# Performance work log

Measured on AMD Instinct MI355X. Metric: run time of the kernel, lower is better.

## Reference

```python
import jax, jax.numpy as jnp
import numpy as np

B, C, L, T = 8, 512, 2048, 64

def setup_inputs() -> dict:
    key = jax.random.key(0)
    k1, k2, k3 = jax.random.split(key, 3)
    x = jax.random.normal(k1, (B, C, 1, L), dtype=jnp.float32)
    W1 = jax.random.normal(k2, (T, C), dtype=jnp.float32) * (1.0 / np.sqrt(C))
    W2 = jax.random.normal(k3, (T, C), dtype=jnp.float32) * (1.0 / np.sqrt(C))
    gamma = jnp.ones((1, 1), dtype=jnp.float32)
    ranges = 0  # unused by forward
    return {"x": x, "W1": W1, "W2": W2, "gamma": gamma, "ranges": ranges}

def reference(x, W1, W2, gamma, ranges):
    temp = x[:, :, 0, :]                                  # (B, C, L)
    q = jnp.einsum('tc,bcl->btl', W1, temp)               # conv1x1 -> (B, T, L)
    k = jnp.einsum('tc,bcl->btl', W2, temp)               # conv1x1 -> (B, T, L)
    scores = jnp.einsum('btl,btm->blm', q, k)             # Q^T K -> (B, L, L)
    attn = jax.nn.softmax(scores, axis=2)                 # softmax over last dim
    # temp @ attn^T: out[:, :, j] = sum_i attn[j, i] * temp[:, :, i]
    out = jnp.einsum('bci,bji->bcj', temp, attn)          # (B, C, L)
    out = temp + gamma[0, 0] * out                        # gamma scale + residual
    return out[:, :, None, :]                             # (B, C, 1, L)
```

## Files before the change

kernel.cpp:

```cpp
#include <hip/hip_runtime.h>
#include <cstddef>

#define BB 8
#define CC 512
#define LL 2048
#define TT 64

typedef short short8 __attribute__((ext_vector_type(8)));
typedef float floatx4 __attribute__((ext_vector_type(4)));
typedef unsigned short b16u;
typedef unsigned int u32;

static __device__ __forceinline__ unsigned f2bfu(float f) {
    unsigned u = __float_as_uint(f);
    u += 0x7fffu + ((u >> 16) & 1u);
    return u >> 16;
}
static __device__ __forceinline__ float bfu2f(unsigned h) {
    return __uint_as_float(h << 16);
}

#define MFMA16(a, b, c) __builtin_amdgcn_mfma_f32_16x16x32_bf16((a), (b), (c), 0, 0, 0)

__global__ __launch_bounds__(256) void wcvt_kernel(
    const float* __restrict__ W1, const float* __restrict__ W2,
    b16u* __restrict__ W1h, b16u* __restrict__ W1l,
    b16u* __restrict__ W2h, b16u* __restrict__ W2l)
{
    int flat = blockIdx.x * 256 + threadIdx.x;
    float4 v1 = *(const float4*)(W1 + (size_t)flat * 4);
    float4 v2 = *(const float4*)(W2 + (size_t)flat * 4);
    const float* e1 = (const float*)&v1;
    const float* e2 = (const float*)&v2;
    unsigned h1[4], l1[4], h2[4], l2[4];
#pragma unroll
    for (int k = 0; k < 4; ++k) {
        h1[k] = f2bfu(e1[k]); l1[k] = f2bfu(e1[k] - bfu2f(h1[k]));
        h2[k] = f2bfu(e2[k]); l2[k] = f2bfu(e2[k] - bfu2f(h2[k]));
    }
    uint2 a, b, c, d;
    a.x = h1[0] | (h1[1] << 16); a.y = h1[2] | (h1[3] << 16);
    b.x = l1[0] | (l1[1] << 16); b.y = l1[2] | (l1[3] << 16);
    c.x = h2[0] | (h2[1] << 16); c.y = h2[2] | (h2[3] << 16);
    d.x = l2[0] | (l2[1] << 16); d.y = l2[2] | (l2[3] << 16);
    *(uint2*)(W1h + (size_t)flat * 4) = a;
    *(uint2*)(W1l + (size_t)flat * 4) = b;
    *(uint2*)(W2h + (size_t)flat * 4) = c;
    *(uint2*)(W2l + (size_t)flat * 4) = d;
}

__global__ __launch_bounds__(256) void qkcvt_kernel(
    const float* __restrict__ x,
    const b16u* __restrict__ W1h, const b16u* __restrict__ W1l,
    const b16u* __restrict__ W2h, const b16u* __restrict__ W2l,
    b16u* __restrict__ Qt, b16u* __restrict__ Kt)
{
    __shared__ b16u Sxh[64 * 72];
    __shared__ b16u Sxl[64 * 72];
    __shared__ b16u S1h[64 * 72];
    __shared__ b16u S1l[64 * 72];
    __shared__ b16u S2h[64 * 72];
    __shared__ b16u S2l[64 * 72];
    const int b  = blockIdx.y;
    const int l0 = blockIdx.x * 64;
    const int tid = threadIdx.x;
    const int lane = tid & 63;
    const int w = tid >> 6;
    const int n16 = lane & 15;
    const int qd = lane >> 4;
    const float* xb = x + (size_t)b * CC * LL;

    const int cx = tid >> 2;
    const int sx = tid & 3;

    float4 xreg[4];
#pragma unroll
    for (int p = 0; p < 4; ++p)
        xreg[p] = *(const float4*)(xb + (size_t)cx * LL + l0 + (sx * 4 + p) * 4);

    floatx4 aq[4], ak[4];
#pragma unroll
    for (int nt = 0; nt < 4; ++nt) {
        aq[nt] = (floatx4){0.f, 0.f, 0.f, 0.f};
        ak[nt] = (floatx4){0.f, 0.f, 0.f, 0.f};
    }

    for (int c0 = 0; c0 < 512; c0 += 64) {
        __syncthreads();
#pragma unroll
        for (int p = 0; p < 4; ++p) {
            const float* e = (const float*)&xreg[p];
            int lbase = (sx * 4 + p) * 4;
#pragma unroll
            for (int k = 0; k < 4; ++k) {
                unsigned h = f2bfu(e[k]);
                unsigned lo = f2bfu(e[k] - bfu2f(h));
                Sxh[(lbase + k) * 72 + cx] = (b16u)h;
                Sxl[(lbase + k) * 72 + cx] = (b16u)lo;
            }
        }
#pragma unroll
        for (int p = 0; p < 2; ++p) {
            int flat = tid + p * 256;
            int t = flat >> 3, s8 = flat & 7;
            size_t off = (size_t)t * 512 + c0 + s8 * 8;
            *(uint4*)&S1h[t * 72 + s8 * 8] = *(const uint4*)(W1h + off);
            *(uint4*)&S1l[t * 72 + s8 * 8] = *(const uint4*)(W1l + off);
            *(uint4*)&S2h[t * 72 + s8 * 8] = *(const uint4*)(W2h + off);
            *(uint4*)&S2l[t * 72 + s8 * 8] = *(const uint4*)(W2l + off);
        }
        __syncthreads();
        if (c0 < 448) {
#pragma unroll
            for (int p = 0; p < 4; ++p)
                xreg[p] = *(const float4*)(xb + (size_t)(c0 + 64 + cx) * LL +
                                           l0 + (sx * 4 + p) * 4);
        }
#pragma unroll
        for (int kc = 0; kc < 2; ++kc) {
            const int ao = (w * 16 + n16) * 72 + kc * 32 + qd * 8;
            short8 a1h = *(const short8*)&S1h[ao];
            short8 a1l = *(const short8*)&S1l[ao];
            short8 a2h = *(const short8*)&S2h[ao];
            short8 a2l = *(const short8*)&S2l[ao];
#pragma unroll
            for (int nt = 0; nt < 4; ++nt) {
                const int bo = (nt * 16 + n16) * 72 + kc * 32 + qd * 8;
                short8 bh = *(const short8*)&Sxh[bo];
                short8 bl = *(const short8*)&Sxl[bo];
                aq[nt] = MFMA16(a1h, bh, aq[nt]);
                aq[nt] = MFMA16(a1h, bl, aq[nt]);
                aq[nt] = MFMA16(a1l, bh, aq[nt]);
                ak[nt] = MFMA16(a2h, bh, ak[nt]);
                ak[nt] = MFMA16(a2h, bl, ak[nt]);
                ak[nt] = MFMA16(a2l, bh, ak[nt]);
            }
        }
    }
#pragma unroll
    for (int nt = 0; nt < 4; ++nt) {
        int l = l0 + nt * 16 + n16;
        uint2 pq, pk;
        pq.x = f2bfu(aq[nt][0]) | (f2bfu(aq[nt][1]) << 16);
        pq.y = f2bfu(aq[nt][2]) | (f2bfu(aq[nt][3]) << 16);
        pk.x = f2bfu(ak[nt][0]) | (f2bfu(ak[nt][1]) << 16);
        pk.y = f2bfu(ak[nt][2]) | (f2bfu(ak[nt][3]) << 16);
        *(uint2*)(Qt + ((size_t)(b * 2048) + l) * 64 + w * 16 + qd * 4) = pq;
        *(uint2*)(Kt + ((size_t)(b * 2048) + l) * 64 + w * 16 + qd * 4) = pk;
    }
}

__global__ __launch_bounds__(256) void xcvt_kernel(
    const float* __restrict__ x, b16u* __restrict__ XT)
{
    int flat = blockIdx.x * 256 + threadIdx.x;
    int i4 = flat & 15;
    int t  = (flat >> 4) & 31;
    int c  = (flat >> 9) & 511;
    int b  = flat >> 18;
    float4 v = *(const float4*)(x + ((size_t)(b * 512 + c)) * 2048 + t * 64 + i4 * 4);
    uint2 wv;
    wv.x = f2bfu(v.x) | (f2bfu(v.y) << 16);
    wv.y = f2bfu(v.z) | (f2bfu(v.w) << 16);
    *(uint2*)(XT + (((size_t)(b * 32) + t) * 512 + c) * 64 + i4 * 4) = wv;
}

__global__ __launch_bounds__(768, 3) void fused_kernel(
    const float* __restrict__ x, const b16u* __restrict__ XT,
    const b16u* __restrict__ Qt, const b16u* __restrict__ Kt,
    const float* __restrict__ gamma, float* __restrict__ out)
{
    __shared__ __align__(16) char smem[140544];
    b16u*  Ps = (b16u*)smem;
    float* Zw = (float*)(smem + 139264);
    float* Zf = (float*)(smem + 140288);

    const int bid = blockIdx.x;
    const int b   = bid & 7;
    const int j0  = (bid >> 3) * 64;
    const int tid = threadIdx.x;
    const int lane = tid & 63;
    const int w    = tid >> 6;
    const int n16  = lane & 15;
    const int qd   = lane >> 4;

    const b16u* Qb = Qt + ((size_t)(b * LL) + j0 + n16) * 64 + qd * 8;
    const b16u* Kb = Kt + ((size_t)(b * LL) + (w & 3) * 16 + n16) * 64 + qd * 8;
    const b16u* Vb = XT + (size_t)b * (32 * 32768) +
                     ((size_t)((w - 4) * 64 + n16)) * 64 + qd * 8;

    short8 qf[4][2];
    short8 kA[2], kB[2];
    float  zacc[4] = {0.f, 0.f, 0.f, 0.f};
    floatx4 acc[4][4];
    short8 av[4][2];

#define KLOAD(KR, T)                                                       \
    {                                                                      \
        const b16u* kp = Kb + (size_t)(T) * 4096;                          \
        KR[0] = *(const short8*)(kp);                                      \
        KR[1] = *(const short8*)(kp + 32);                                 \
    }

#define VLOAD(T)                                                           \
    {                                                                      \
        const b16u* vp = Vb + (size_t)(T) * 32768;                         \
        _Pragma("unroll")                                                  \
        for (int mt = 0; mt < 4; ++mt) {                                   \
            av[mt][0] = *(const short8*)(vp + mt * 1024);                  \
            av[mt][1] = *(const short8*)(vp + mt * 1024 + 32);             \
        }                                                                  \
    }

#define SSTEP(PSOFF, KR)                                                   \
    {                                                                      \
        _Pragma("unroll")                                                  \
        for (int nt = 0; nt < 4; ++nt) {                                   \
            floatx4 sacc = (floatx4){0.f, 0.f, 0.f, 0.f};                  \
            sacc = MFMA16(KR[0], qf[nt][0], sacc);                         \
            sacc = MFMA16(KR[1], qf[nt][1], sacc);                         \
            float p0 = __expf(sacc[0] - 20.0f);                            \
            float p1 = __expf(sacc[1] - 20.0f);                            \
            float p2 = __expf(sacc[2] - 20.0f);                            \
            float p3 = __expf(sacc[3] - 20.0f);                            \
            zacc[nt] += (p0 + p1) + (p2 + p3);                             \
            uint2 pk;                                                      \
            pk.x = f2bfu(p0) | (f2bfu(p1) << 16);                          \
            pk.y = f2bfu(p2) | (f2bfu(p3) << 16);                          \
            int jl = nt * 16 + n16;                                        \
            int phys = ((w & 3) * 2 + (qd >> 1)) ^ (n16 & 7);              \
            *(uint2*)&Ps[(PSOFF) + jl * 64 + phys * 8 + (qd & 1) * 4] = pk;\
        }                                                                  \
    }

#define PVSTEP(PSOFF)                                                      \
    {                                                                      \
        __builtin_amdgcn_s_setprio(1);                                     \
        _Pragma("unroll")                                                  \
        for (int kc = 0; kc < 2; ++kc) {                                   \
            short8 bfr[4];                                                 \
            _Pragma("unroll")                                              \
            for (int nt = 0; nt < 4; ++nt) {                               \
                int phys = (kc * 4 + qd) ^ (n16 & 7);                      \
                bfr[nt] = *(const short8*)&Ps[(PSOFF) +                    \
                    (nt * 16 + n16) * 64 + phys * 8];                      \
            }                                                              \
            _Pragma("unroll")                                              \
            for (int mt = 0; mt < 4; ++mt)                                 \
                _Pragma("unroll")                                          \
                for (int nt = 0; nt < 4; ++nt)                             \
                    acc[mt][nt] = MFMA16(av[mt][kc], bfr[nt], acc[mt][nt]);\
        }                                                                  \
        __builtin_amdgcn_s_setprio(0);                                     \
    }

    if (w < 4) {
#pragma unroll
        for (int nt = 0; nt < 4; ++nt) {
            qf[nt][0] = *(const short8*)(Qb + nt * 1024);
            qf[nt][1] = *(const short8*)(Qb + nt * 1024 + 32);
        }
        KLOAD(kA, 0)
        SSTEP(0, kA)
        KLOAD(kA, 1)
    } else {
#pragma unroll
        for (int mt = 0; mt < 4; ++mt)
#pragma unroll
            for (int nt = 0; nt < 4; ++nt)
                acc[mt][nt] = (floatx4){0.f, 0.f, 0.f, 0.f};
        VLOAD(0)
    }
    __syncthreads();

    for (int tt = 0; tt < 32; tt += 2) {
        if (w < 4) {
            SSTEP(4096, kA)
            if (tt + 2 < 32) KLOAD(kB, tt + 2)
        } else {
            PVSTEP(0)
            VLOAD(tt + 1)
        }
        __syncthreads();
        if (w < 4) {
            if (tt + 2 < 32) {
                SSTEP(0, kB)
                if (tt + 3 < 32) KLOAD(kA, tt + 3)
            }
        } else {
            PVSTEP(4096)
            if (tt + 2 < 32) VLOAD(tt + 2)
        }
        __syncthreads();
    }
#undef KLOAD
#undef VLOAD
#undef SSTEP
#undef PVSTEP

    if (w < 4) {
#pragma unroll
        for (int nt = 0; nt < 4; ++nt) {
            float z = zacc[nt];
            z += __shfl_xor(z, 16);
            z += __shfl_xor(z, 32);
            if (qd == 0) Zw[w * 64 + nt * 16 + n16] = z;
        }
    }
    __syncthreads();
    if (tid < 64)
        Zf[tid] = Zw[tid] + Zw[64 + tid] + Zw[128 + tid] + Zw[192 + tid];
    __syncthreads();

    const float g = gamma[0];
    if (w >= 4) {
        float* st = (float*)(smem + (w - 4) * 17408);
#pragma unroll
        for (int nt = 0; nt < 4; ++nt) {
            float zi = g / Zf[nt * 16 + n16];
#pragma unroll
            for (int mt = 0; mt < 4; ++mt)
#pragma unroll
                for (int r = 0; r < 4; ++r)
                    st[(mt * 16 + qd * 4 + r) * 68 + nt * 16 + n16] =
                        acc[mt][nt][r] * zi;
        }
    }
    __syncthreads();
    if (w >= 4) {
        const float* st = (const float*)(smem + (w - 4) * 17408);
#pragma unroll
        for (int p = 0; p < 16; ++p) {
            int rl = qd * 16 + p;
            int cg = (w - 4) * 64 + rl;
            size_t go = ((size_t)(b * CC) + cg) * 2048 + j0 + n16 * 4;
            float4 v = *(const float4*)&st[rl * 68 + n16 * 4];
            float4 xv = *(const float4*)(x + go);
            v.x += xv.x; v.y += xv.y; v.z += xv.z; v.w += xv.w;
            *(float4*)(out + go) = v;
        }
    }
}

extern "C" void kernel_launch(void* const* d_in, const int* in_sizes, int n_in,
                              void* d_out, int out_size, void* d_ws, size_t ws_size,
                              hipStream_t stream)
{
    (void)in_sizes; (void)n_in; (void)out_size; (void)ws_size;
    const float* x     = (const float*)d_in[0];
    const float* W1    = (const float*)d_in[1];
    const float* W2    = (const float*)d_in[2];
    const float* gamma = (const float*)d_in[3];
    float* out = (float*)d_out;

    b16u* Qt  = (b16u*)d_ws;
    b16u* Kt  = Qt  + (size_t)BB * LL * TT;
    b16u* W1h = Kt  + (size_t)BB * LL * TT;
    b16u* W1l = W1h + (size_t)TT * CC;
    b16u* W2h = W1l + (size_t)TT * CC;
    b16u* W2l = W2h + (size_t)TT * CC;
    b16u* XT  = W2l + (size_t)TT * CC;

    wcvt_kernel <<<dim3(32),      256, 0, stream>>>(W1, W2, W1h, W1l, W2h, W2l);
    xcvt_kernel <<<dim3(8192),    256, 0, stream>>>(x, XT);
    qkcvt_kernel<<<dim3(32, BB),  256, 0, stream>>>(x, W1h, W1l, W2h, W2l, Qt, Kt);
    fused_kernel<<<dim3(256),     768, 0, stream>>>(x, XT, Qt, Kt, gamma, out);
}
```

Measured before the change: 205.5 us.

## Split channels across blocks, drop warp specialization, fuse x conversion into QK prep

Folds the separate x-to-bf16 transpose kernel into the Q/K projection kernel, which already reads x. The fused attention kernel changes from 768-thread warp-specialized blocks (score warps vs PV warps) to 512-thread blocks where every warp computes both scores and PV. It also splits the channel dimension in half across twice as many blocks, with much less shared memory so more blocks fit per CU. Softmax now uses exp2 with LOG2E folded into Q and the shift folded into the accumulator init, plus packed bf16 conversion. The trade-off is that scores are recomputed for each channel half and the epilogue uses uncoalesced scalar stores.

```diff
diff --git a/kernel.cpp b/kernel.cpp
--- a/kernel.cpp
+++ b/kernel.cpp
@@ -10,6 +10,9 @@
 typedef float floatx4 __attribute__((ext_vector_type(4)));
 typedef unsigned short b16u;
 typedef unsigned int u32;
+
+#define LOG2E 1.44269504088896f
+#define NEG20LOG2E -28.8539008177793f
 
 static __device__ __forceinline__ unsigned f2bfu(float f) {
     unsigned u = __float_as_uint(f);
@@ -49,11 +52,11 @@
     *(uint2*)(W2l + (size_t)flat * 4) = d;
 }
 
-__global__ __launch_bounds__(256) void qkcvt_kernel(
+__global__ __launch_bounds__(256) void prep_kernel(
     const float* __restrict__ x,
     const b16u* __restrict__ W1h, const b16u* __restrict__ W1l,
     const b16u* __restrict__ W2h, const b16u* __restrict__ W2l,
-    b16u* __restrict__ Qt, b16u* __restrict__ Kt)
+    b16u* __restrict__ Qt, b16u* __restrict__ Kt, b16u* __restrict__ XT)
 {
     __shared__ b16u Sxh[64 * 72];
     __shared__ b16u Sxl[64 * 72];
@@ -62,7 +65,8 @@
     __shared__ b16u S2h[64 * 72];
     __shared__ b16u S2l[64 * 72];
     const int b  = blockIdx.y;
-    const int l0 = blockIdx.x * 64;
+    const int lt = blockIdx.x;
+    const int l0 = lt * 64;
     const int tid = threadIdx.x;
     const int lane = tid & 63;
     const int w = tid >> 6;
@@ -91,13 +95,19 @@
         for (int p = 0; p < 4; ++p) {
             const float* e = (const float*)&xreg[p];
             int lbase = (sx * 4 + p) * 4;
+            unsigned hh[4];
 #pragma unroll
             for (int k = 0; k < 4; ++k) {
                 unsigned h = f2bfu(e[k]);
                 unsigned lo = f2bfu(e[k] - bfu2f(h));
+                hh[k] = h;
                 Sxh[(lbase + k) * 72 + cx] = (b16u)h;
                 Sxl[(lbase + k) * 72 + cx] = (b16u)lo;
             }
+            uint2 wv;
+            wv.x = hh[0] | (hh[1] << 16);
+            wv.y = hh[2] | (hh[3] << 16);
+            *(uint2*)(XT + (((size_t)(b * 32) + lt) * 512 + c0 + cx) * 64 + lbase) = wv;
         }
 #pragma unroll
         for (int p = 0; p < 2; ++p) {
@@ -141,8 +151,8 @@
     for (int nt = 0; nt < 4; ++nt) {
         int l = l0 + nt * 16 + n16;
         uint2 pq, pk;
-        pq.x = f2bfu(aq[nt][0]) | (f2bfu(aq[nt][1]) << 16);
-        pq.y = f2bfu(aq[nt][2]) | (f2bfu(aq[nt][3]) << 16);
+        pq.x = f2bfu(aq[nt][0] * LOG2E) | (f2bfu(aq[nt][1] * LOG2E) << 16);
+        pq.y = f2bfu(aq[nt][2] * LOG2E) | (f2bfu(aq[nt][3] * LOG2E) << 16);
         pk.x = f2bfu(ak[nt][0]) | (f2bfu(ak[nt][1]) << 16);
         pk.y = f2bfu(ak[nt][2]) | (f2bfu(ak[nt][3]) << 16);
         *(uint2*)(Qt + ((size_t)(b * 2048) + l) * 64 + w * 16 + qd * 4) = pq;
@@ -150,50 +160,50 @@
     }
 }
 
-__global__ __launch_bounds__(256) void xcvt_kernel(
-    const float* __restrict__ x, b16u* __restrict__ XT)
-{
-    int flat = blockIdx.x * 256 + threadIdx.x;
-    int i4 = flat & 15;
-    int t  = (flat >> 4) & 31;
-    int c  = (flat >> 9) & 511;
-    int b  = flat >> 18;
-    float4 v = *(const float4*)(x + ((size_t)(b * 512 + c)) * 2048 + t * 64 + i4 * 4);
-    uint2 wv;
-    wv.x = f2bfu(v.x) | (f2bfu(v.y) << 16);
-    wv.y = f2bfu(v.z) | (f2bfu(v.w) << 16);
-    *(uint2*)(XT + (((size_t)(b * 32) + t) * 512 + c) * 64 + i4 * 4) = wv;
-}
-
-__global__ __launch_bounds__(768, 3) void fused_kernel(
+__global__ __launch_bounds__(512, 4) void fused_kernel(
     const float* __restrict__ x, const b16u* __restrict__ XT,
     const b16u* __restrict__ Qt, const b16u* __restrict__ Kt,
     const float* __restrict__ gamma, float* __restrict__ out)
 {
-    __shared__ __align__(16) char smem[140544];
+    __shared__ __align__(16) char smem[17664];
     b16u*  Ps = (b16u*)smem;
-    float* Zw = (float*)(smem + 139264);
-    float* Zf = (float*)(smem + 140288);
+    float* Zw = (float*)(smem + 16384);
+    float* Zf = (float*)(smem + 17408);
 
     const int bid = blockIdx.x;
     const int b   = bid & 7;
-    const int j0  = (bid >> 3) * 64;
+    const int jt  = (bid >> 3) & 31;
+    const int ch  = bid >> 8;
+    const int j0  = jt * 64;
+    const int c0  = ch * 256;
     const int tid = threadIdx.x;
     const int lane = tid & 63;
     const int w    = tid >> 6;
     const int n16  = lane & 15;
     const int qd   = lane >> 4;
-
-    const b16u* Qb = Qt + ((size_t)(b * LL) + j0 + n16) * 64 + qd * 8;
-    const b16u* Kb = Kt + ((size_t)(b * LL) + (w & 3) * 16 + n16) * 64 + qd * 8;
+    const int si   = w & 3;
+    const int sj   = w >> 2;
+
+    const b16u* Qb = Qt + ((size_t)(b * LL) + j0 + sj * 32 + n16) * 64 + qd * 8;
+    const b16u* Kb = Kt + ((size_t)(b * LL) + si * 16 + n16) * 64 + qd * 8;
     const b16u* Vb = XT + (size_t)b * (32 * 32768) +
-                     ((size_t)((w - 4) * 64 + n16)) * 64 + qd * 8;
-
-    short8 qf[4][2];
-    short8 kA[2], kB[2];
-    float  zacc[4] = {0.f, 0.f, 0.f, 0.f};
-    floatx4 acc[4][4];
-    short8 av[4][2];
+                     (size_t)(c0 + w * 32 + n16) * 64 + qd * 8;
+
+    short8 qf[2][2];
+#pragma unroll
+    for (int nt = 0; nt < 2; ++nt)
+#pragma unroll
+        for (int kc = 0; kc < 2; ++kc)
+            qf[nt][kc] = *(const short8*)(Qb + nt * 1024 + kc * 32);
+
+    floatx4 acc[2][4];
+#pragma unroll
+    for (int mt = 0; mt < 2; ++mt)
+#pragma unroll
+        for (int nt = 0; nt < 4; ++nt) acc[mt][nt] = (floatx4){0.f, 0.f, 0.f, 0.f};
+    float zacc[2] = {0.f, 0.f};
+
+    short8 kA[2], kB[2], av[2][2];
 
 #define KLOAD(KR, T)                                                       \
     {                                                                      \
@@ -206,7 +216,7 @@
     {                                                                      \
         const b16u* vp = Vb + (size_t)(T) * 32768;                         \
         _Pragma("unroll")                                                  \
-        for (int mt = 0; mt < 4; ++mt) {                                   \
+        for (int mt = 0; mt < 2; ++mt) {                                   \
             av[mt][0] = *(const short8*)(vp + mt * 1024);                  \
             av[mt][1] = *(const short8*)(vp + mt * 1024 + 32);             \
         }                                                                  \
@@ -215,27 +225,29 @@
 #define SSTEP(PSOFF, KR)                                                   \
     {                                                                      \
         _Pragma("unroll")                                                  \
-        for (int nt = 0; nt < 4; ++nt) {                                   \
-            floatx4 sacc = (floatx4){0.f, 0.f, 0.f, 0.f};                  \
+        for (int nt = 0; nt < 2; ++nt) {                                   \
+            floatx4 sacc = (floatx4){NEG20LOG2E, NEG20LOG2E,               \
+                                     NEG20LOG2E, NEG20LOG2E};              \
             sacc = MFMA16(KR[0], qf[nt][0], sacc);                         \
             sacc = MFMA16(KR[1], qf[nt][1], sacc);                         \
-            float p0 = __expf(sacc[0] - 20.0f);                            \
-            float p1 = __expf(sacc[1] - 20.0f);                            \
-            float p2 = __expf(sacc[2] - 20.0f);                            \
-            float p3 = __expf(sacc[3] - 20.0f);                            \
+            float p0 = __builtin_amdgcn_exp2f(sacc[0]);                    \
+            float p1 = __builtin_amdgcn_exp2f(sacc[1]);                    \
+            float p2 = __builtin_amdgcn_exp2f(sacc[2]);                    \
+            float p3 = __builtin_amdgcn_exp2f(sacc[3]);                    \
             zacc[nt] += (p0 + p1) + (p2 + p3);                             \
             uint2 pk;                                                      \
-            pk.x = f2bfu(p0) | (f2bfu(p1) << 16);                          \
-            pk.y = f2bfu(p2) | (f2bfu(p3) << 16);                          \
-            int jl = nt * 16 + n16;                                        \
-            int phys = ((w & 3) * 2 + (qd >> 1)) ^ (n16 & 7);              \
+            asm("v_cvt_pk_bf16_f32 %0, %1, %2" : "=v"(pk.x)                \
+                : "v"(p0), "v"(p1));                                       \
+            asm("v_cvt_pk_bf16_f32 %0, %1, %2" : "=v"(pk.y)                \
+                : "v"(p2), "v"(p3));                                       \
+            int jl = sj * 32 + nt * 16 + n16;                              \
+            int phys = (si * 2 + (qd >> 1)) ^ (n16 & 7);                   \
             *(uint2*)&Ps[(PSOFF) + jl * 64 + phys * 8 + (qd & 1) * 4] = pk;\
         }                                                                  \
     }
 
 #define PVSTEP(PSOFF)                                                      \
     {                                                                      \
-        __builtin_amdgcn_s_setprio(1);                                     \
         _Pragma("unroll")                                                  \
         for (int kc = 0; kc < 2; ++kc) {                                   \
             short8 bfr[4];                                                 \
@@ -246,51 +258,28 @@
                     (nt * 16 + n16) * 64 + phys * 8];                      \
             }                                                              \
             _Pragma("unroll")                                              \
-            for (int mt = 0; mt < 4; ++mt)                                 \
+            for (int mt = 0; mt < 2; ++mt)                                 \
                 _Pragma("unroll")                                          \
                 for (int nt = 0; nt < 4; ++nt)                             \
                     acc[mt][nt] = MFMA16(av[mt][kc], bfr[nt], acc[mt][nt]);\
         }                                                                  \
-        __builtin_amdgcn_s_setprio(0);                                     \
-    }
-
-    if (w < 4) {
-#pragma unroll
-        for (int nt = 0; nt < 4; ++nt) {
-            qf[nt][0] = *(const short8*)(Qb + nt * 1024);
-            qf[nt][1] = *(const short8*)(Qb + nt * 1024 + 32);
-        }
-        KLOAD(kA, 0)
-        SSTEP(0, kA)
-        KLOAD(kA, 1)
-    } else {
-#pragma unroll
-        for (int mt = 0; mt < 4; ++mt)
-#pragma unroll
-            for (int nt = 0; nt < 4; ++nt)
-                acc[mt][nt] = (floatx4){0.f, 0.f, 0.f, 0.f};
-        VLOAD(0)
-    }
+    }
+
+    KLOAD(kA, 0)
+    SSTEP(0, kA)
+    KLOAD(kB, 1)
     __syncthreads();
 
     for (int tt = 0; tt < 32; tt += 2) {
-        if (w < 4) {
-            SSTEP(4096, kA)
-            if (tt + 2 < 32) KLOAD(kB, tt + 2)
-        } else {
-            PVSTEP(0)
-            VLOAD(tt + 1)
-        }
+        VLOAD(tt)
+        SSTEP(4096, kB)
+        if (tt + 2 < 32) KLOAD(kA, tt + 2)
+        PVSTEP(0)
         __syncthreads();
-        if (w < 4) {
-            if (tt + 2 < 32) {
-                SSTEP(0, kB)
-                if (tt + 3 < 32) KLOAD(kA, tt + 3)
-            }
-        } else {
-            PVSTEP(4096)
-            if (tt + 2 < 32) VLOAD(tt + 2)
-        }
+        VLOAD(tt + 1)
+        if (tt + 2 < 32) SSTEP(0, kA)
+        if (tt + 3 < 32) KLOAD(kB, tt + 3)
+        PVSTEP(4096)
         __syncthreads();
     }
 #undef KLOAD
@@ -298,47 +287,33 @@
 #undef SSTEP
 #undef PVSTEP
 
-    if (w < 4) {
-#pragma unroll
-        for (int nt = 0; nt < 4; ++nt) {
-            float z = zacc[nt];
-            z += __shfl_xor(z, 16);
-            z += __shfl_xor(z, 32);
-            if (qd == 0) Zw[w * 64 + nt * 16 + n16] = z;
-        }
+#pragma unroll
+    for (int nt = 0; nt < 2; ++nt) {
+        float z = zacc[nt];
+        z += __shfl_xor(z, 16);
+        z += __shfl_xor(z, 32);
+        if (qd == 0) Zw[w * 32 + nt * 16 + n16] = z;
     }
     __syncthreads();
-    if (tid < 64)
-        Zf[tid] = Zw[tid] + Zw[64 + tid] + Zw[128 + tid] + Zw[192 + tid];
+    if (tid < 64) {
+        int sjj = tid >> 5, v = tid & 31;
+        Zf[tid] = Zw[(sjj * 4 + 0) * 32 + v] + Zw[(sjj * 4 + 1) * 32 + v] +
+                  Zw[(sjj * 4 + 2) * 32 + v] + Zw[(sjj * 4 + 3) * 32 + v];
+    }
     __syncthreads();
 
     const float g = gamma[0];
-    if (w >= 4) {
-        float* st = (float*)(smem + (w - 4) * 17408);
-#pragma unroll
-        for (int nt = 0; nt < 4; ++nt) {
-            float zi = g / Zf[nt * 16 + n16];
-#pragma unroll
-            for (int mt = 0; mt < 4; ++mt)
-#pragma unroll
-                for (int r = 0; r < 4; ++r)
-                    st[(mt * 16 + qd * 4 + r) * 68 + nt * 16 + n16] =
-                        acc[mt][nt][r] * zi;
-        }
-    }
-    __syncthreads();
-    if (w >= 4) {
-        const float* st = (const float*)(smem + (w - 4) * 17408);
-#pragma unroll
-        for (int p = 0; p < 16; ++p) {
-            int rl = qd * 16 + p;
-            int cg = (w - 4) * 64 + rl;
-            size_t go = ((size_t)(b * CC) + cg) * 2048 + j0 + n16 * 4;
-            float4 v = *(const float4*)&st[rl * 68 + n16 * 4];
-            float4 xv = *(const float4*)(x + go);
-            v.x += xv.x; v.y += xv.y; v.z += xv.z; v.w += xv.w;
-            *(float4*)(out + go) = v;
-        }
+#pragma unroll
+    for (int nt = 0; nt < 4; ++nt) {
+        float zi = g / Zf[nt * 16 + n16];
+#pragma unroll
+        for (int mt = 0; mt < 2; ++mt)
+#pragma unroll
+            for (int r = 0; r < 4; ++r) {
+                int cg = c0 + w * 32 + mt * 16 + qd * 4 + r;
+                size_t go = ((size_t)(b * CC) + cg) * 2048 + j0 + nt * 16 + n16;
+                out[go] = x[go] + acc[mt][nt][r] * zi;
+            }
     }
 }
 
@@ -361,8 +336,8 @@
     b16u* W2l = W2h + (size_t)TT * CC;
     b16u* XT  = W2l + (size_t)TT * CC;
 
-    wcvt_kernel <<<dim3(32),      256, 0, stream>>>(W1, W2, W1h, W1l, W2h, W2l);
-    xcvt_kernel <<<dim3(8192),    256, 0, stream>>>(x, XT);
-    qkcvt_kernel<<<dim3(32, BB),  256, 0, stream>>>(x, W1h, W1l, W2h, W2l, Qt, Kt);
-    fused_kernel<<<dim3(256),     768, 0, stream>>>(x, XT, Qt, Kt, gamma, out);
-}
+    wcvt_kernel<<<dim3(32),     256, 0, stream>>>(W1, W2, W1h, W1l, W2h, W2l);
+    prep_kernel<<<dim3(32, BB), 256, 0, stream>>>(x, W1h, W1l, W2h, W2l,
+                                                  Qt, Kt, XT);
+    fused_kernel<<<dim3(512),   512, 0, stream>>>(x, XT, Qt, Kt, gamma, out);
+}
```

Result: faster. 197.5 us (-3.9%).
